# Optimization experiments

Hardware: AMD Instinct MI355X
Metric: run time of the kernel (lower is better)

Reference implementation:

```python
import jax, jax.numpy as jnp
import numpy as np

B, N, D = 8, 4096, 512
NUM_CODES = 8192

def setup_inputs() -> dict:
    key = jax.random.key(0)
    kx, kc = jax.random.split(key)
    x = jax.random.normal(kx, (B, N, D), dtype=jnp.float32)
    codebook = jax.random.normal(kc, (NUM_CODES, D), dtype=jnp.float32)
    return {"x": x, "codebook": codebook}

def reference(x, codebook):
    # x: (B, N, D); codebook: (K, D)
    b = x.shape[0]
    flat = x.reshape(-1, x.shape[-1])  # (B*N, D)
    distances = (
        jnp.sum(flat * flat, axis=1, keepdims=True)
        + jnp.sum(codebook * codebook, axis=1)
        - 2.0 * flat @ codebook.T
    )
    codes = jnp.argmin(distances, axis=1).reshape(b, -1)  # (B, N) int
    return codes
```

## Files before the change

kernel.cpp:

```cpp
#include <hip/hip_runtime.h>
#include <hip/hip_bf16.h>
#include <hip/hip_fp16.h>


#define M_ROWS 32768
#define DDIM   512
#define KCODES 8192
#define NCAND  8

typedef unsigned long long u64;
typedef unsigned int u32;
typedef __attribute__((ext_vector_type(4))) float f32x4;
typedef __attribute__((ext_vector_type(8))) int v8i;

#define GL2LDS(gp, lp) __builtin_amdgcn_global_load_lds(                  \
    (const __attribute__((address_space(1))) void*)(gp),                  \
    (__attribute__((address_space(3))) void*)(lp), 16, 0, 0)

__device__ __forceinline__ u32 umin32(u32 a, u32 b) { return a < b ? a : b; }
__device__ __forceinline__ u32 umax32(u32 a, u32 b) { return a > b ? a : b; }
__device__ __forceinline__ u64 umin64(u64 a, u64 b) { return a < b ? a : b; }
__device__ __forceinline__ u32 umin3(u32 a, u32 b, u32 c) {
  return umin32(umin32(a, b), c);
}
__device__ __forceinline__ u32 med3u(u32 a, u32 b, u32 c) {
  u32 d;
  asm("v_med3_u32 %0, %1, %2, %3" : "=v"(d) : "v"(a), "v"(b), "v"(c));
  return d;
}

__device__ __forceinline__ u32 fsort(float s) {
  u32 fb = __float_as_uint(s);
  return fb ^ (u32)(((int)fb >> 31) | 0x80000000);
}

__device__ __forceinline__ uint2 pk8_fp8(float4 v0, float4 v1) {
  int lo = 0, hi = 0;
  lo = __builtin_amdgcn_cvt_pk_fp8_f32(v0.x, v0.y, lo, false);
  lo = __builtin_amdgcn_cvt_pk_fp8_f32(v0.z, v0.w, lo, true);
  hi = __builtin_amdgcn_cvt_pk_fp8_f32(v1.x, v1.y, hi, false);
  hi = __builtin_amdgcn_cvt_pk_fp8_f32(v1.z, v1.w, hi, true);
  return (uint2){(u32)lo, (u32)hi};
}

__global__ __launch_bounds__(256) void conv_codebook_kernel(
    const float* __restrict__ cb, unsigned char* __restrict__ ch8,
    float* __restrict__ cnh) {
  int wave = (blockIdx.x * 256 + threadIdx.x) >> 6;
  int lane = threadIdx.x & 63;
  if (wave >= KCODES) return;
  const float* src = cb + (size_t)wave * DDIM + lane * 8;
  float4 v0 = *(const float4*)(src);
  float4 v1 = *(const float4*)(src + 4);
  *(uint2*)(ch8 + (size_t)wave * DDIM + lane * 8) = pk8_fp8(v0, v1);
  float ss = v0.x*v0.x + v0.y*v0.y + v0.z*v0.z + v0.w*v0.w
           + v1.x*v1.x + v1.y*v1.y + v1.z*v1.z + v1.w*v1.w;
#pragma unroll
  for (int off = 32; off; off >>= 1) ss += __shfl_xor(ss, off);
  if (lane == 0) cnh[wave] = 0.5f * ss;
}

__global__ __launch_bounds__(256) void conv_x_kernel(
    const float* __restrict__ x, unsigned char* __restrict__ xh8) {
  size_t i = ((size_t)blockIdx.x * 256 + threadIdx.x) * 8;
  float4 v0 = *(const float4*)(x + i);
  float4 v1 = *(const float4*)(x + i + 4);
  *(uint2*)(xh8 + i) = pk8_fp8(v0, v1);
}

__global__ __launch_bounds__(512, 4) void coarse_kernel(
    const unsigned char* __restrict__ xh8, const unsigned char* __restrict__ ch8,
    const float* __restrict__ cnh, uint4* __restrict__ part) {
  __shared__ __align__(16) char smem[65536];
  uint2* tab = (uint2*)smem;

  const int tid  = threadIdx.x;
  const int lane = tid & 63;
  const int wid  = tid >> 6;
  const int wm   = wid >> 2, wn = wid & 3;
  const int g    = lane >> 4, l16 = lane & 15;

  const int xcd  = blockIdx.x & 7;
  const int lid  = blockIdx.x >> 3;
  const int nblk = lid >> 5;
  const int mblk = (xcd << 5) | (lid & 31);
  const int row0 = mblk * 128;
  const int col0 = nblk * 128;

  const int a_ = lane >> 3, b_ = lane & 7;
  const size_t gsrc = (size_t)a_ * DDIM + ((b_ ^ a_) << 4);
  const unsigned char* abase = xh8 + (size_t)row0 * DDIM + gsrc;
  const unsigned char* bbase = ch8 + (size_t)col0 * DDIM + gsrc;

  const int sl0 = (((g * 2) ^ (l16 & 7)) << 4);
  const int slX = sl0 ^ 16;
  const int aoff = (wm * 64 + l16) * 128;
  const int boff = (wn * 32 + l16) * 128;

#define STAGE(cc, buf) do {                                               \
    char* sa_ = smem + (buf) * 32768;                                     \
    _Pragma("unroll")                                                     \
    for (int j = 0; j < 2; ++j) {                                         \
      const int I_ = wid * 2 + j;                                         \
      const size_t off_ = (size_t)(I_ * 8) * DDIM + (size_t)(cc) * 128;   \
      GL2LDS(abase + off_, sa_ + I_ * 1024);                              \
      GL2LDS(bbase + off_, sa_ + 16384 + I_ * 1024);                      \
    }                                                                     \
  } while (0)

  u32 codev[2];
  float cn[2];
#pragma unroll
  for (int tn = 0; tn < 2; ++tn) {
    codev[tn] = (u32)(col0 + wn * 32 + tn * 16 + l16);
    cn[tn] = cnh[codev[tn]];
  }

  f32x4 acc[4][2];
#pragma unroll
  for (int tm = 0; tm < 4; ++tm)
#pragma unroll
    for (int tn = 0; tn < 2; ++tn) acc[tm][tn] = (f32x4){0.f, 0.f, 0.f, 0.f};

  STAGE(0, 0);
  __syncthreads();

#pragma unroll
  for (int c = 0; c < 4; ++c) {
    if (c < 3) STAGE(c + 1, (c + 1) & 1);
    const char* aL = smem + (c & 1) * 32768;
    const char* bL = aL + 16384;
    const char* paL = aL + aoff + sl0;
    const char* paH = aL + aoff + slX;
    const char* pbL = bL + boff + sl0;
    const char* pbH = bL + boff + slX;

    v8i af[4];
#pragma unroll
    for (int t = 0; t < 4; ++t) {
      int4 lo = *(const int4*)(paL + t * 2048);
      int4 hi = *(const int4*)(paH + t * 2048);
      af[t][0] = lo.x; af[t][1] = lo.y; af[t][2] = lo.z; af[t][3] = lo.w;
      af[t][4] = hi.x; af[t][5] = hi.y; af[t][6] = hi.z; af[t][7] = hi.w;
    }
#pragma unroll
    for (int tn = 0; tn < 2; ++tn) {
      int4 lo = *(const int4*)(pbL + tn * 2048);
      int4 hi = *(const int4*)(pbH + tn * 2048);
      v8i bf;
      bf[0] = lo.x; bf[1] = lo.y; bf[2] = lo.z; bf[3] = lo.w;
      bf[4] = hi.x; bf[5] = hi.y; bf[6] = hi.z; bf[7] = hi.w;
#pragma unroll
      for (int tm = 0; tm < 4; ++tm)
        acc[tm][tn] = __builtin_amdgcn_mfma_scale_f32_16x16x128_f8f6f4(
            af[tm], bf, acc[tm][tn],
            0, 0,
            0, 0x7F7F7F7F,
            0, 0x7F7F7F7F);
    }
    __syncthreads();
  }

  u32 k1[16], k2[16];
#pragma unroll
  for (int tm = 0; tm < 4; ++tm)
#pragma unroll
    for (int r = 0; r < 4; ++r) {
      const int sl = tm * 4 + r;
      float s0 = cn[0] - acc[tm][0][r];
      float s1 = cn[1] - acc[tm][1][r];
      u32 key0 = (__float_as_uint(s0) & 0xFFFFE000u) | codev[0];
      u32 key1 = (__float_as_uint(s1) & 0xFFFFE000u) | codev[1];
      k1[sl] = umin32(key0, key1);
      k2[sl] = umax32(key0, key1);
    }

  u32 m1 = ~0u, m2 = ~0u, m3 = ~0u;
#pragma unroll
  for (int p = 0; p < 4; ++p) {
    __syncthreads();
    if (wn == p) {
#pragma unroll
      for (int tm = 0; tm < 4; ++tm)
#pragma unroll
        for (int r = 0; r < 4; ++r) {
          const int row = wm * 64 + tm * 16 + g * 4 + r;
          const int sl = tm * 4 + r;
          tab[row * 17 + l16] = (uint2){k1[sl], k2[sl]};
        }
    }
    __syncthreads();
    if (tid < 128) {
#pragma unroll
      for (int e = 0; e < 16; ++e) {
        uint2 v = tab[tid * 17 + e];
        u32 a = umax32(m1, v.x);
        m1 = umin32(m1, v.x);
        u32 b = med3u(m2, a, v.y);
        m2 = umin3(m2, a, v.y);
        m3 = umin32(m3, b);
      }
    }
  }

  if (tid < 128)
    part[(size_t)nblk * M_ROWS + row0 + tid] = (uint4){m1, m2, m3, 0u};
#undef STAGE
}

__global__ __launch_bounds__(256) void merge_kernel(
    const uint4* __restrict__ part, int* __restrict__ cand) {
  const int row = blockIdx.x * 256 + threadIdx.x;
  u32 k[NCAND];
#pragma unroll
  for (int i = 0; i < NCAND; ++i) k[i] = ~0u;
  for (int nb = 0; nb < KCODES / 128; ++nb) {
    uint4 e = part[(size_t)nb * M_ROWS + row];
    u32 t = e.x;
#pragma unroll
    for (int i = 0; i < NCAND; ++i) { u32 mx = umax32(k[i], t); k[i] = umin32(k[i], t); t = mx; }
    t = e.y;
#pragma unroll
    for (int i = 0; i < NCAND; ++i) { u32 mx = umax32(k[i], t); k[i] = umin32(k[i], t); t = mx; }
    t = e.z;
#pragma unroll
    for (int i = 0; i < NCAND; ++i) { u32 mx = umax32(k[i], t); k[i] = umin32(k[i], t); t = mx; }
  }
#pragma unroll
  for (int i = 0; i < NCAND; ++i)
    cand[row * NCAND + i] = (int)(k[i] & 0x1FFFu);
}

__global__ __launch_bounds__(256) void rescore_kernel(
    const float* __restrict__ x, const float* __restrict__ cb,
    const float* __restrict__ cnh, const int* __restrict__ cand,
    int* __restrict__ out) {
  int wave = (blockIdx.x * 256 + threadIdx.x) >> 6;
  int lane = threadIdx.x & 63;
  if (wave >= M_ROWS) return;
  int idx[NCAND];
#pragma unroll
  for (int j = 0; j < NCAND; ++j) idx[j] = cand[wave * NCAND + j];

  const float* xr = x + (size_t)wave * DDIM + lane * 8;
  float4 x0 = *(const float4*)(xr);
  float4 x1 = *(const float4*)(xr + 4);

  float d[NCAND];
#pragma unroll
  for (int j = 0; j < NCAND; ++j) {
    const float* c = cb + (size_t)idx[j] * DDIM + lane * 8;
    float4 a0 = *(const float4*)(c);
    float4 a1 = *(const float4*)(c + 4);
    d[j] = x0.x*a0.x + x0.y*a0.y + x0.z*a0.z + x0.w*a0.w
         + x1.x*a1.x + x1.y*a1.y + x1.z*a1.z + x1.w*a1.w;
  }
#pragma unroll
  for (int off = 32; off; off >>= 1)
#pragma unroll
    for (int j = 0; j < NCAND; ++j) d[j] += __shfl_xor(d[j], off);

  if (lane == 0) {
    u64 best = ~0ull;
#pragma unroll
    for (int j = 0; j < NCAND; ++j) {
      float s = cnh[idx[j]] - d[j];
      u64 key = ((u64)fsort(s) << 32) | (u32)idx[j];
      best = umin64(best, key);
    }
    out[wave] = (int)(u32)best;
  }
}

extern "C" void kernel_launch(void* const* d_in, const int* in_sizes, int n_in,
                              void* d_out, int out_size, void* d_ws, size_t ws_size,
                              hipStream_t stream) {
  const float* x  = (const float*)d_in[0];
  const float* cb = (const float*)d_in[1];
  int* out = (int*)d_out;

  char* ws = (char*)d_ws;
  unsigned char* ch8  = (unsigned char*)(ws);
  unsigned char* xh8  = (unsigned char*)(ws + (size_t)4 * 1024 * 1024);
  float*         cnh  = (float*)(ws + (size_t)20 * 1024 * 1024);
  int*           cand = (int*)(ws + (size_t)20 * 1024 * 1024 + 32 * 1024);
  uint4*         part = (uint4*)(ws + (size_t)22 * 1024 * 1024);

  conv_codebook_kernel<<<KCODES / 4, 256, 0, stream>>>(cb, ch8, cnh);
  conv_x_kernel<<<(M_ROWS * DDIM) / (256 * 8), 256, 0, stream>>>(x, xh8);
  coarse_kernel<<<(M_ROWS / 128) * (KCODES / 128), 512, 0, stream>>>(xh8, ch8, cnh, part);
  merge_kernel<<<M_ROWS / 256, 256, 0, stream>>>(part, cand);
  rescore_kernel<<<M_ROWS / 4, 256, 0, stream>>>(x, cb, cnh, cand, out);
}
```

Measured before the change: 373.4 us.

## Keep x tile in registers and stream codebook tiles in persistent coarse blocks

The coarse kernel now loads each block's 128-row x fragment once into registers and loops over 16 codebook chunks of 64 codes, staging only the codebook through double-buffered LDS. The grid shrinks from 16384 to 2048 blocks, with each block covering 1024 codes, and partial top-3 results are written per 256 codes, so merge reads half as many partials. This removes repeated A-tile staging and cuts launch count and partial traffic. In exchange it adds register pressure from the held A fragments, more barriers per iteration, and less parallelism.

```diff
diff --git a/kernel.cpp b/kernel.cpp
--- a/kernel.cpp
+++ b/kernel.cpp
@@ -71,141 +71,129 @@
 __global__ __launch_bounds__(512, 4) void coarse_kernel(
     const unsigned char* __restrict__ xh8, const unsigned char* __restrict__ ch8,
     const float* __restrict__ cnh, uint4* __restrict__ part) {
-  __shared__ __align__(16) char smem[65536];
-  uint2* tab = (uint2*)smem;
+  __shared__ __align__(16) char smem[33792];
+  uint2* tab = (uint2*)(smem + 16384);
 
   const int tid  = threadIdx.x;
   const int lane = tid & 63;
   const int wid  = tid >> 6;
-  const int wm   = wid >> 2, wn = wid & 3;
+  const int wm   = wid >> 1, wn = wid & 1;
   const int g    = lane >> 4, l16 = lane & 15;
 
-  const int xcd  = blockIdx.x & 7;
-  const int lid  = blockIdx.x >> 3;
-  const int nblk = lid >> 5;
-  const int mblk = (xcd << 5) | (lid & 31);
+  const int mblk = blockIdx.x >> 3;
+  const int ngrp = blockIdx.x & 7;
   const int row0 = mblk * 128;
-  const int col0 = nblk * 128;
-
-  const int a_ = lane >> 3, b_ = lane & 7;
-  const size_t gsrc = (size_t)a_ * DDIM + ((b_ ^ a_) << 4);
-  const unsigned char* abase = xh8 + (size_t)row0 * DDIM + gsrc;
-  const unsigned char* bbase = ch8 + (size_t)col0 * DDIM + gsrc;
-
-  const int sl0 = (((g * 2) ^ (l16 & 7)) << 4);
-  const int slX = sl0 ^ 16;
-  const int aoff = (wm * 64 + l16) * 128;
-  const int boff = (wn * 32 + l16) * 128;
-
-#define STAGE(cc, buf) do {                                               \
-    char* sa_ = smem + (buf) * 32768;                                     \
-    _Pragma("unroll")                                                     \
-    for (int j = 0; j < 2; ++j) {                                         \
-      const int I_ = wid * 2 + j;                                         \
-      const size_t off_ = (size_t)(I_ * 8) * DDIM + (size_t)(cc) * 128;   \
-      GL2LDS(abase + off_, sa_ + I_ * 1024);                              \
-      GL2LDS(bbase + off_, sa_ + 16384 + I_ * 1024);                      \
-    }                                                                     \
-  } while (0)
-
-  u32 codev[2];
-  float cn[2];
-#pragma unroll
-  for (int tn = 0; tn < 2; ++tn) {
-    codev[tn] = (u32)(col0 + wn * 32 + tn * 16 + l16);
-    cn[tn] = cnh[codev[tn]];
-  }
-
-  f32x4 acc[4][2];
-#pragma unroll
-  for (int tm = 0; tm < 4; ++tm)
-#pragma unroll
-    for (int tn = 0; tn < 2; ++tn) acc[tm][tn] = (f32x4){0.f, 0.f, 0.f, 0.f};
-
-  STAGE(0, 0);
+  const int colgrp = ngrp * 1024;
+
+  v8i A[2][4];
+#pragma unroll
+  for (int tm = 0; tm < 2; ++tm) {
+    const unsigned char* ap =
+        xh8 + (size_t)(row0 + wm * 32 + tm * 16 + l16) * DDIM + g * 32;
+#pragma unroll
+    for (int c = 0; c < 4; ++c) {
+      int4 lo = *(const int4*)(ap + c * 128);
+      int4 hi = *(const int4*)(ap + c * 128 + 16);
+      A[tm][c][0] = lo.x; A[tm][c][1] = lo.y; A[tm][c][2] = lo.z; A[tm][c][3] = lo.w;
+      A[tm][c][4] = hi.x; A[tm][c][5] = hi.y; A[tm][c][6] = hi.z; A[tm][c][7] = hi.w;
+    }
+  }
+
+  const int scode = tid >> 3;
+  const int sgran = (tid & 7) ^ (scode & 7);
+  const unsigned char* bsrc =
+      ch8 + (size_t)(colgrp + scode) * DDIM + sgran * 16;
+
+  const int brow = wn * 32 + l16;
+  const int bsl  = ((g * 2) ^ (l16 & 7)) << 4;
+  const int boff = brow * 128 + bsl;
+
+  u32 m1 = ~0u, m2 = ~0u, m3 = ~0u;
+
+  GL2LDS(bsrc, smem + tid * 16);
   __syncthreads();
 
-#pragma unroll
-  for (int c = 0; c < 4; ++c) {
-    if (c < 3) STAGE(c + 1, (c + 1) & 1);
-    const char* aL = smem + (c & 1) * 32768;
-    const char* bL = aL + 16384;
-    const char* paL = aL + aoff + sl0;
-    const char* paH = aL + aoff + slX;
-    const char* pbL = bL + boff + sl0;
-    const char* pbH = bL + boff + slX;
-
-    v8i af[4];
-#pragma unroll
-    for (int t = 0; t < 4; ++t) {
-      int4 lo = *(const int4*)(paL + t * 2048);
-      int4 hi = *(const int4*)(paH + t * 2048);
-      af[t][0] = lo.x; af[t][1] = lo.y; af[t][2] = lo.z; af[t][3] = lo.w;
-      af[t][4] = hi.x; af[t][5] = hi.y; af[t][6] = hi.z; af[t][7] = hi.w;
-    }
+  for (int nb = 0; nb < 16; ++nb) {
+    const int col0 = colgrp + nb * 64;
+    u32 codev[2];
+    float cn[2];
 #pragma unroll
     for (int tn = 0; tn < 2; ++tn) {
-      int4 lo = *(const int4*)(pbL + tn * 2048);
-      int4 hi = *(const int4*)(pbH + tn * 2048);
-      v8i bf;
-      bf[0] = lo.x; bf[1] = lo.y; bf[2] = lo.z; bf[3] = lo.w;
-      bf[4] = hi.x; bf[5] = hi.y; bf[6] = hi.z; bf[7] = hi.w;
-#pragma unroll
-      for (int tm = 0; tm < 4; ++tm)
-        acc[tm][tn] = __builtin_amdgcn_mfma_scale_f32_16x16x128_f8f6f4(
-            af[tm], bf, acc[tm][tn],
-            0, 0,
-            0, 0x7F7F7F7F,
-            0, 0x7F7F7F7F);
-    }
-    __syncthreads();
-  }
-
-  u32 k1[16], k2[16];
-#pragma unroll
-  for (int tm = 0; tm < 4; ++tm)
-#pragma unroll
-    for (int r = 0; r < 4; ++r) {
-      const int sl = tm * 4 + r;
-      float s0 = cn[0] - acc[tm][0][r];
-      float s1 = cn[1] - acc[tm][1][r];
-      u32 key0 = (__float_as_uint(s0) & 0xFFFFE000u) | codev[0];
-      u32 key1 = (__float_as_uint(s1) & 0xFFFFE000u) | codev[1];
-      k1[sl] = umin32(key0, key1);
-      k2[sl] = umax32(key0, key1);
-    }
-
-  u32 m1 = ~0u, m2 = ~0u, m3 = ~0u;
-#pragma unroll
-  for (int p = 0; p < 4; ++p) {
-    __syncthreads();
-    if (wn == p) {
-#pragma unroll
-      for (int tm = 0; tm < 4; ++tm)
-#pragma unroll
-        for (int r = 0; r < 4; ++r) {
-          const int row = wm * 64 + tm * 16 + g * 4 + r;
-          const int sl = tm * 4 + r;
-          tab[row * 17 + l16] = (uint2){k1[sl], k2[sl]};
+      codev[tn] = (u32)(col0 + wn * 32 + tn * 16 + l16);
+      cn[tn] = cnh[codev[tn]];
+    }
+
+    f32x4 acc[2][2];
+#pragma unroll
+    for (int tm = 0; tm < 2; ++tm)
+#pragma unroll
+      for (int tn = 0; tn < 2; ++tn) acc[tm][tn] = (f32x4){0.f, 0.f, 0.f, 0.f};
+
+#pragma unroll
+    for (int c = 0; c < 4; ++c) {
+      if (c < 3)
+        GL2LDS(bsrc + (c + 1) * 128, smem + ((c + 1) & 1) * 8192 + tid * 16);
+      else if (nb < 15)
+        GL2LDS(bsrc + 32768, smem + tid * 16);
+
+      const char* bL = smem + (c & 1) * 8192;
+#pragma unroll
+      for (int tn = 0; tn < 2; ++tn) {
+        int4 lo = *(const int4*)(bL + boff + tn * 2048);
+        int4 hi = *(const int4*)(bL + ((boff + tn * 2048) ^ 16));
+        v8i bf;
+        bf[0] = lo.x; bf[1] = lo.y; bf[2] = lo.z; bf[3] = lo.w;
+        bf[4] = hi.x; bf[5] = hi.y; bf[6] = hi.z; bf[7] = hi.w;
+#pragma unroll
+        for (int tm = 0; tm < 2; ++tm)
+          acc[tm][tn] = __builtin_amdgcn_mfma_scale_f32_16x16x128_f8f6f4(
+              A[tm][c], bf, acc[tm][tn],
+              0, 0,
+              0, 0x7F7F7F7F,
+              0, 0x7F7F7F7F);
+      }
+      __syncthreads();
+    }
+
+#pragma unroll
+    for (int p = 0; p < 2; ++p) {
+      if (wn == p) {
+#pragma unroll
+        for (int tm = 0; tm < 2; ++tm)
+#pragma unroll
+          for (int r = 0; r < 4; ++r) {
+            float s0 = cn[0] - acc[tm][0][r];
+            float s1 = cn[1] - acc[tm][1][r];
+            u32 key0 = (__float_as_uint(s0) & 0xFFFFE000u) | codev[0];
+            u32 key1 = (__float_as_uint(s1) & 0xFFFFE000u) | codev[1];
+            const int row = wm * 32 + tm * 16 + g * 4 + r;
+            tab[row * 17 + l16] = (uint2){umin32(key0, key1), umax32(key0, key1)};
+          }
+      }
+      __syncthreads();
+      if (tid < 128) {
+#pragma unroll
+        for (int e = 0; e < 16; ++e) {
+          uint2 v = tab[tid * 17 + e];
+          u32 a = umax32(m1, v.x);
+          m1 = umin32(m1, v.x);
+          u32 b = med3u(m2, a, v.y);
+          m2 = umin3(m2, a, v.y);
+          m3 = umin32(m3, b);
         }
-    }
-    __syncthreads();
-    if (tid < 128) {
-#pragma unroll
-      for (int e = 0; e < 16; ++e) {
-        uint2 v = tab[tid * 17 + e];
-        u32 a = umax32(m1, v.x);
-        m1 = umin32(m1, v.x);
-        u32 b = med3u(m2, a, v.y);
-        m2 = umin3(m2, a, v.y);
-        m3 = umin32(m3, b);
-      }
-    }
-  }
-
-  if (tid < 128)
-    part[(size_t)nblk * M_ROWS + row0 + tid] = (uint4){m1, m2, m3, 0u};
-#undef STAGE
+      }
+      __syncthreads();
+    }
+
+    if ((nb & 3) == 3) {
+      if (tid < 128) {
+        part[(size_t)(ngrp * 4 + (nb >> 2)) * M_ROWS + row0 + tid] =
+            (uint4){m1, m2, m3, 0u};
+        m1 = ~0u; m2 = ~0u; m3 = ~0u;
+      }
+    }
+    bsrc += 32768;
+  }
 }
 
 __global__ __launch_bounds__(256) void merge_kernel(
@@ -214,7 +202,7 @@
   u32 k[NCAND];
 #pragma unroll
   for (int i = 0; i < NCAND; ++i) k[i] = ~0u;
-  for (int nb = 0; nb < KCODES / 128; ++nb) {
+  for (int nb = 0; nb < KCODES / 256; ++nb) {
     uint4 e = part[(size_t)nb * M_ROWS + row];
     u32 t = e.x;
 #pragma unroll
@@ -288,7 +276,7 @@
 
   conv_codebook_kernel<<<KCODES / 4, 256, 0, stream>>>(cb, ch8, cnh);
   conv_x_kernel<<<(M_ROWS * DDIM) / (256 * 8), 256, 0, stream>>>(x, xh8);
-  coarse_kernel<<<(M_ROWS / 128) * (KCODES / 128), 512, 0, stream>>>(xh8, ch8, cnh, part);
+  coarse_kernel<<<(M_ROWS / 128) * 8, 512, 0, stream>>>(xh8, ch8, cnh, part);
   merge_kernel<<<M_ROWS / 256, 256, 0, stream>>>(part, cand);
   rescore_kernel<<<M_ROWS / 4, 256, 0, stream>>>(x, cb, cnh, cand, out);
 }
```

New measurement: 367.7 us. No clear change (-1.5%).
